# Performance work log

Hardware: AMD Instinct MI355X
Metric: run time of the kernel (lower is better)

The kernel has to match this reference:

```python
import jax, jax.numpy as jnp
import numpy as np

N_ENTRIES = 4_194_304   # total CSR entries (gene observations)
H, W = 256, 256
N_PIXELS = H * W
N_GENES = 30000
FEATURE_DIM = 64


def setup_inputs() -> dict:
    key = jax.random.key(0)
    k1, k2, k3, k4 = jax.random.split(key, 4)
    # gene id per CSR entry
    indices = jax.random.randint(k1, (N_ENTRIES,), 0, N_GENES, dtype=jnp.int64)
    # counts per entry (positive floats)
    cnts = jax.random.uniform(k2, (N_ENTRIES,), dtype=jnp.float32) * 10.0
    # CSR row pointers over pixels: sorted, starting at 0, ending at N_ENTRIES
    indptr = jnp.sort(jax.random.randint(k3, (N_PIXELS + 1,), 0, N_ENTRIES + 1, dtype=jnp.int64))
    indptr = indptr.at[0].set(0).at[-1].set(N_ENTRIES)
    # params: gamma init zeros, tokens variance_scaling(1.0,'fan_in','normal',out_axis=0)
    gamma = jnp.zeros((N_GENES,), jnp.float32)
    tokens = jax.random.normal(k4, (N_GENES, FEATURE_DIM), dtype=jnp.float32) * (1.0 / np.sqrt(FEATURE_DIM))
    return {"indices": indices, "cnts": cnts, "indptr": indptr, "gamma": gamma, "tokens": tokens}


def reference(indices, cnts, indptr, gamma, tokens):
    # SGStem with rescale=True, normalize=False (module defaults)
    n_entries = indices.shape[0]
    n_pixels = indptr.shape[0] - 1  # == H*W
    # mask padding entries beyond indptr[-1]
    valid = jnp.arange(n_entries) < indptr[-1]
    c = jnp.where(valid, cnts, 0.0)
    # rescale counts by per-gene exp(gamma)
    c = c * jnp.exp(gamma[indices])
    # CSR -> segment ids per entry
    rpt = jnp.diff(indptr)
    segms = jnp.repeat(jnp.arange(n_pixels), rpt, total_repeat_length=n_entries)
    # gather token embeddings, scale, scatter-add into pixel bins
    embeddings = tokens[indices] * c[:, None]  # (n_entries, feature_dim)
    embedding_sum = jax.ops.segment_sum(embeddings, segms, num_segments=n_pixels)
    return embedding_sum.reshape(H, W, tokens.shape[-1])
```

## Files before the change

kernel.cpp:

```cpp
#include <hip/hip_runtime.h>
#include <hip/hip_bf16.h>

#define FDIM 64
#define N_PIXELS 65536
#define N_ENTRIES 4194304
#define EPW 512
#define N_WAVES (N_ENTRIES / EPW)
#define PAD 64

typedef unsigned int u32;
typedef u32 u32x4 __attribute__((ext_vector_type(4)));

__device__ __forceinline__ unsigned short f32_to_bf16_rne(float f) {
    unsigned int u = __float_as_uint(f);
    u = (u + 0x7FFFu + ((u >> 16) & 1u)) >> 16;
    return (unsigned short)u;
}

__global__ __launch_bounds__(256) void convert_tokens(
    const float4* __restrict__ tokens4,
    const float* __restrict__ gamma,
    ushort4* __restrict__ tok_bf)
{
    const int i = blockIdx.x * blockDim.x + threadIdx.x;
    const int g = i >> 4;
    const float eg = __expf(gamma[g]);
    const float4 t = tokens4[i];
    ushort4 o;
    o.x = f32_to_bf16_rne(t.x * eg);
    o.y = f32_to_bf16_rne(t.y * eg);
    o.z = f32_to_bf16_rne(t.z * eg);
    o.w = f32_to_bf16_rne(t.w * eg);
    tok_bf[i] = o;
}

__global__ __launch_bounds__(64) void search_starts(
    const int* __restrict__ indptr,
    int* __restrict__ p0arr)
{
    const int w = blockIdx.x * 64 + threadIdx.x;
    const int e0 = w * EPW;
    int lo = 0, hi = N_PIXELS;
    while (lo < hi) {
        const int mid = (lo + hi + 1) >> 1;
        if (indptr[mid] <= e0) lo = mid; else hi = mid - 1;
    }
    p0arr[w] = lo;
}

__global__ __launch_bounds__(64, 4) void sgstem_main(
    const int* __restrict__ indices,
    const float* __restrict__ cnts,
    const int* __restrict__ indptr,
    const char* __restrict__ tokp,
    const int* __restrict__ p0arr,
    float* __restrict__ out)
{
    __shared__ int2 meta[EPW + PAD];

    const int lane = threadIdx.x;
    const int g    = lane >> 3;
    const int fl   = lane & 7;
    const int flb  = fl * 16;

    const int wid = __builtin_amdgcn_readfirstlane(blockIdx.x);
    const int e0 = wid * EPW;
    const int e1 = e0 + EPW;

    #pragma unroll
    for (int c = 0; c < EPW / 64; ++c) {
        const int e = e0 + c * 64 + lane;
        const int   idx = indices[e];
        const float cnt = cnts[e];
        meta[c * 64 + lane] = make_int2(idx * 128, __float_as_int(cnt));
    }
    meta[EPW + lane] = make_int2(0, 0);

    int p = p0arr[wid];

    #define GLOAD(dst, off) \
        asm volatile("global_load_dwordx4 %0, %1, %2" \
                     : "=v"(dst) : "v"(off), "s"(tokp) : "memory")
    #define CONSUME(tk, sc) \
        a0 = fmaf(__uint_as_float(tk.x << 16),         sc, a0); \
        a1 = fmaf(__uint_as_float(tk.x & 0xFFFF0000u), sc, a1); \
        a2 = fmaf(__uint_as_float(tk.y << 16),         sc, a2); \
        a3 = fmaf(__uint_as_float(tk.y & 0xFFFF0000u), sc, a3); \
        a4 = fmaf(__uint_as_float(tk.z << 16),         sc, a4); \
        a5 = fmaf(__uint_as_float(tk.z & 0xFFFF0000u), sc, a5); \
        a6 = fmaf(__uint_as_float(tk.w << 16),         sc, a6); \
        a7 = fmaf(__uint_as_float(tk.w & 0xFFFF0000u), sc, a7)

    while (p < N_PIXELS) {
        const int ps = indptr[p];
        if (ps >= e1) break;
        const int pe = indptr[p + 1];
        const int s = max(ps, e0);
        const int t = min(pe, e1);

        if (t > s) {
            const int r0 = s - e0;
            const int r1 = t - e0;

            float a0 = 0.f, a1 = 0.f, a2 = 0.f, a3 = 0.f;
            float a4 = 0.f, a5 = 0.f, a6 = 0.f, a7 = 0.f;

            int rb = r0;
            for (; rb + 64 <= r1; rb += 64) {
                const int q = rb + g;
                const int2 m0 = meta[q];
                const int2 m1 = meta[q + 8];
                const int2 m2 = meta[q + 16];
                const int2 m3 = meta[q + 24];
                const int2 m4 = meta[q + 32];
                const int2 m5 = meta[q + 40];
                const int2 m6 = meta[q + 48];
                const int2 m7 = meta[q + 56];

                u32x4 t0, t1, t2, t3, t4, t5, t6, t7;
                GLOAD(t0, m0.x + flb); GLOAD(t1, m1.x + flb);
                GLOAD(t2, m2.x + flb); GLOAD(t3, m3.x + flb);
                GLOAD(t4, m4.x + flb); GLOAD(t5, m5.x + flb);
                GLOAD(t6, m6.x + flb); GLOAD(t7, m7.x + flb);

                const float s0 = __int_as_float(m0.y);
                const float s1 = __int_as_float(m1.y);
                const float s2 = __int_as_float(m2.y);
                const float s3 = __int_as_float(m3.y);
                const float s4 = __int_as_float(m4.y);
                const float s5 = __int_as_float(m5.y);
                const float s6 = __int_as_float(m6.y);
                const float s7 = __int_as_float(m7.y);

                asm volatile("s_waitcnt vmcnt(4)" ::: "memory");
                __builtin_amdgcn_sched_barrier(0);
                CONSUME(t0, s0); CONSUME(t1, s1); CONSUME(t2, s2); CONSUME(t3, s3);
                asm volatile("s_waitcnt vmcnt(0)" ::: "memory");
                __builtin_amdgcn_sched_barrier(0);
                CONSUME(t4, s4); CONSUME(t5, s5); CONSUME(t6, s6); CONSUME(t7, s7);
            }

            if (rb < r1) {
                const int q = rb + g;
                const int2 m0 = meta[q];
                const int2 m1 = meta[q + 8];
                const int2 m2 = meta[q + 16];
                const int2 m3 = meta[q + 24];
                const int2 m4 = meta[q + 32];
                const int2 m5 = meta[q + 40];
                const int2 m6 = meta[q + 48];
                const int2 m7 = meta[q + 56];

                const int o0 = ((q      < r1) ? m0.x : 0) + flb;
                const int o1 = ((q +  8 < r1) ? m1.x : 0) + flb;
                const int o2 = ((q + 16 < r1) ? m2.x : 0) + flb;
                const int o3 = ((q + 24 < r1) ? m3.x : 0) + flb;
                const int o4 = ((q + 32 < r1) ? m4.x : 0) + flb;
                const int o5 = ((q + 40 < r1) ? m5.x : 0) + flb;
                const int o6 = ((q + 48 < r1) ? m6.x : 0) + flb;
                const int o7 = ((q + 56 < r1) ? m7.x : 0) + flb;

                u32x4 t0, t1, t2, t3, t4, t5, t6, t7;
                GLOAD(t0, o0); GLOAD(t1, o1); GLOAD(t2, o2); GLOAD(t3, o3);
                GLOAD(t4, o4); GLOAD(t5, o5); GLOAD(t6, o6); GLOAD(t7, o7);

                const float s0 = (q      < r1) ? __int_as_float(m0.y) : 0.f;
                const float s1 = (q +  8 < r1) ? __int_as_float(m1.y) : 0.f;
                const float s2 = (q + 16 < r1) ? __int_as_float(m2.y) : 0.f;
                const float s3 = (q + 24 < r1) ? __int_as_float(m3.y) : 0.f;
                const float s4 = (q + 32 < r1) ? __int_as_float(m4.y) : 0.f;
                const float s5 = (q + 40 < r1) ? __int_as_float(m5.y) : 0.f;
                const float s6 = (q + 48 < r1) ? __int_as_float(m6.y) : 0.f;
                const float s7 = (q + 56 < r1) ? __int_as_float(m7.y) : 0.f;

                asm volatile("s_waitcnt vmcnt(4)" ::: "memory");
                __builtin_amdgcn_sched_barrier(0);
                CONSUME(t0, s0); CONSUME(t1, s1); CONSUME(t2, s2); CONSUME(t3, s3);
                asm volatile("s_waitcnt vmcnt(0)" ::: "memory");
                __builtin_amdgcn_sched_barrier(0);
                CONSUME(t4, s4); CONSUME(t5, s5); CONSUME(t6, s6); CONSUME(t7, s7);
            }

            #pragma unroll
            for (int mask = 8; mask <= 32; mask <<= 1) {
                a0 += __shfl_xor(a0, mask);
                a1 += __shfl_xor(a1, mask);
                a2 += __shfl_xor(a2, mask);
                a3 += __shfl_xor(a3, mask);
                a4 += __shfl_xor(a4, mask);
                a5 += __shfl_xor(a5, mask);
                a6 += __shfl_xor(a6, mask);
                a7 += __shfl_xor(a7, mask);
            }

            if (g == 0) {
                const bool interior = (ps >= e0) && (pe <= e1);
                if (interior) {
                    float4* o4 = (float4*)(out + p * FDIM);
                    o4[fl * 2]     = make_float4(a0, a1, a2, a3);
                    o4[fl * 2 + 1] = make_float4(a4, a5, a6, a7);
                } else {
                    float* o = out + p * FDIM + fl * 8;
                    atomicAdd(o + 0, a0);
                    atomicAdd(o + 1, a1);
                    atomicAdd(o + 2, a2);
                    atomicAdd(o + 3, a3);
                    atomicAdd(o + 4, a4);
                    atomicAdd(o + 5, a5);
                    atomicAdd(o + 6, a6);
                    atomicAdd(o + 7, a7);
                }
            }
        }
        ++p;
    }
    #undef GLOAD
    #undef CONSUME
}

extern "C" void kernel_launch(void* const* d_in, const int* in_sizes, int n_in,
                              void* d_out, int out_size, void* d_ws, size_t ws_size,
                              hipStream_t stream) {
    const int*    indices = (const int*)d_in[0];
    const float*  cnts    = (const float*)d_in[1];
    const int*    indptr  = (const int*)d_in[2];
    const float*  gamma   = (const float*)d_in[3];
    const float4* tokens4 = (const float4*)d_in[4];
    float*        out     = (float*)d_out;

    int*     p0arr  = (int*)d_ws;
    ushort4* tok_bf = (ushort4*)((char*)d_ws + 32768);

    hipMemsetAsync(d_out, 0, (size_t)N_PIXELS * FDIM * sizeof(float), stream);

    convert_tokens<<<1875, 256, 0, stream>>>(tokens4, gamma, tok_bf);
    search_starts<<<N_WAVES / 64, 64, 0, stream>>>(indptr, p0arr);

    sgstem_main<<<N_WAVES, 64, 0, stream>>>(
        indices, cnts, indptr, (const char*)tok_bf, p0arr, out);
}
```

Baseline: 153.1 us.

## Software-pipeline token gathers across chunks and pixels with double-buffered register sets

Restructures the per-wave loop into a flat chunk stream, where each chunk is up to 64 entries of one pixel. Two register sets (A/B) are used so the next chunk's eight gather loads are issued before the current chunk is consumed, including across pixel boundaries. The aim is to hide global-load latency that the old per-pixel loop exposed at each pixel's start. The cost is doubled register use for loaded tokens, which may lower occupancy, plus more complex control flow.

```diff
diff --git a/kernel.cpp b/kernel.cpp
--- a/kernel.cpp
+++ b/kernel.cpp
@@ -70,17 +70,59 @@
     #pragma unroll
     for (int c = 0; c < EPW / 64; ++c) {
         const int e = e0 + c * 64 + lane;
-        const int   idx = indices[e];
-        const float cnt = cnts[e];
-        meta[c * 64 + lane] = make_int2(idx * 128, __float_as_int(cnt));
+        meta[c * 64 + lane] = make_int2(indices[e] * 128, __float_as_int(cnts[e]));
     }
     meta[EPW + lane] = make_int2(0, 0);
 
-    int p = p0arr[wid];
+    int cp = p0arr[wid], cps = 0, cpe = 0, crb = 0, cr1 = 0;
+    {
+        bool found = false;
+        while (cp < N_PIXELS) {
+            const int ps = indptr[cp];
+            if (ps >= e1) break;
+            const int pe = indptr[cp + 1];
+            const int s = max(ps, e0), t = min(pe, e1);
+            if (t > s) { cps = ps; cpe = pe; crb = s - e0; cr1 = t - e0; found = true; break; }
+            ++cp;
+        }
+        if (!found) return;
+    }
+
+    u32x4 tA0, tA1, tA2, tA3, tA4, tA5, tA6, tA7;
+    u32x4 tB0, tB1, tB2, tB3, tB4, tB5, tB6, tB7;
+    float sA0, sA1, sA2, sA3, sA4, sA5, sA6, sA7;
+    float sB0, sB1, sB2, sB3, sB4, sB5, sB6, sB7;
+    float a0 = 0.f, a1 = 0.f, a2 = 0.f, a3 = 0.f;
+    float a4 = 0.f, a5 = 0.f, a6 = 0.f, a7 = 0.f;
 
     #define GLOAD(dst, off) \
         asm volatile("global_load_dwordx4 %0, %1, %2" \
                      : "=v"(dst) : "v"(off), "s"(tokp) : "memory")
+
+    #define ISSUE(SET, RB, R1) do { \
+        const int q_ = (RB) + g; \
+        const int2 m0_ = meta[q_];      const int2 m1_ = meta[q_ + 8]; \
+        const int2 m2_ = meta[q_ + 16]; const int2 m3_ = meta[q_ + 24]; \
+        const int2 m4_ = meta[q_ + 32]; const int2 m5_ = meta[q_ + 40]; \
+        const int2 m6_ = meta[q_ + 48]; const int2 m7_ = meta[q_ + 56]; \
+        GLOAD(t##SET##0, ((q_      < (R1)) ? m0_.x : 0) + flb); \
+        GLOAD(t##SET##1, ((q_ +  8 < (R1)) ? m1_.x : 0) + flb); \
+        GLOAD(t##SET##2, ((q_ + 16 < (R1)) ? m2_.x : 0) + flb); \
+        GLOAD(t##SET##3, ((q_ + 24 < (R1)) ? m3_.x : 0) + flb); \
+        GLOAD(t##SET##4, ((q_ + 32 < (R1)) ? m4_.x : 0) + flb); \
+        GLOAD(t##SET##5, ((q_ + 40 < (R1)) ? m5_.x : 0) + flb); \
+        GLOAD(t##SET##6, ((q_ + 48 < (R1)) ? m6_.x : 0) + flb); \
+        GLOAD(t##SET##7, ((q_ + 56 < (R1)) ? m7_.x : 0) + flb); \
+        s##SET##0 = (q_      < (R1)) ? __int_as_float(m0_.y) : 0.f; \
+        s##SET##1 = (q_ +  8 < (R1)) ? __int_as_float(m1_.y) : 0.f; \
+        s##SET##2 = (q_ + 16 < (R1)) ? __int_as_float(m2_.y) : 0.f; \
+        s##SET##3 = (q_ + 24 < (R1)) ? __int_as_float(m3_.y) : 0.f; \
+        s##SET##4 = (q_ + 32 < (R1)) ? __int_as_float(m4_.y) : 0.f; \
+        s##SET##5 = (q_ + 40 < (R1)) ? __int_as_float(m5_.y) : 0.f; \
+        s##SET##6 = (q_ + 48 < (R1)) ? __int_as_float(m6_.y) : 0.f; \
+        s##SET##7 = (q_ + 56 < (R1)) ? __int_as_float(m7_.y) : 0.f; \
+    } while (0)
+
     #define CONSUME(tk, sc) \
         a0 = fmaf(__uint_as_float(tk.x << 16),         sc, a0); \
         a1 = fmaf(__uint_as_float(tk.x & 0xFFFF0000u), sc, a1); \
@@ -91,131 +133,93 @@
         a6 = fmaf(__uint_as_float(tk.w << 16),         sc, a6); \
         a7 = fmaf(__uint_as_float(tk.w & 0xFFFF0000u), sc, a7)
 
-    while (p < N_PIXELS) {
-        const int ps = indptr[p];
-        if (ps >= e1) break;
-        const int pe = indptr[p + 1];
-        const int s = max(ps, e0);
-        const int t = min(pe, e1);
-
-        if (t > s) {
-            const int r0 = s - e0;
-            const int r1 = t - e0;
-
-            float a0 = 0.f, a1 = 0.f, a2 = 0.f, a3 = 0.f;
-            float a4 = 0.f, a5 = 0.f, a6 = 0.f, a7 = 0.f;
-
-            int rb = r0;
-            for (; rb + 64 <= r1; rb += 64) {
-                const int q = rb + g;
-                const int2 m0 = meta[q];
-                const int2 m1 = meta[q + 8];
-                const int2 m2 = meta[q + 16];
-                const int2 m3 = meta[q + 24];
-                const int2 m4 = meta[q + 32];
-                const int2 m5 = meta[q + 40];
-                const int2 m6 = meta[q + 48];
-                const int2 m7 = meta[q + 56];
-
-                u32x4 t0, t1, t2, t3, t4, t5, t6, t7;
-                GLOAD(t0, m0.x + flb); GLOAD(t1, m1.x + flb);
-                GLOAD(t2, m2.x + flb); GLOAD(t3, m3.x + flb);
-                GLOAD(t4, m4.x + flb); GLOAD(t5, m5.x + flb);
-                GLOAD(t6, m6.x + flb); GLOAD(t7, m7.x + flb);
-
-                const float s0 = __int_as_float(m0.y);
-                const float s1 = __int_as_float(m1.y);
-                const float s2 = __int_as_float(m2.y);
-                const float s3 = __int_as_float(m3.y);
-                const float s4 = __int_as_float(m4.y);
-                const float s5 = __int_as_float(m5.y);
-                const float s6 = __int_as_float(m6.y);
-                const float s7 = __int_as_float(m7.y);
-
-                asm volatile("s_waitcnt vmcnt(4)" ::: "memory");
-                __builtin_amdgcn_sched_barrier(0);
-                CONSUME(t0, s0); CONSUME(t1, s1); CONSUME(t2, s2); CONSUME(t3, s3);
-                asm volatile("s_waitcnt vmcnt(0)" ::: "memory");
-                __builtin_amdgcn_sched_barrier(0);
-                CONSUME(t4, s4); CONSUME(t5, s5); CONSUME(t6, s6); CONSUME(t7, s7);
-            }
-
-            if (rb < r1) {
-                const int q = rb + g;
-                const int2 m0 = meta[q];
-                const int2 m1 = meta[q + 8];
-                const int2 m2 = meta[q + 16];
-                const int2 m3 = meta[q + 24];
-                const int2 m4 = meta[q + 32];
-                const int2 m5 = meta[q + 40];
-                const int2 m6 = meta[q + 48];
-                const int2 m7 = meta[q + 56];
-
-                const int o0 = ((q      < r1) ? m0.x : 0) + flb;
-                const int o1 = ((q +  8 < r1) ? m1.x : 0) + flb;
-                const int o2 = ((q + 16 < r1) ? m2.x : 0) + flb;
-                const int o3 = ((q + 24 < r1) ? m3.x : 0) + flb;
-                const int o4 = ((q + 32 < r1) ? m4.x : 0) + flb;
-                const int o5 = ((q + 40 < r1) ? m5.x : 0) + flb;
-                const int o6 = ((q + 48 < r1) ? m6.x : 0) + flb;
-                const int o7 = ((q + 56 < r1) ? m7.x : 0) + flb;
-
-                u32x4 t0, t1, t2, t3, t4, t5, t6, t7;
-                GLOAD(t0, o0); GLOAD(t1, o1); GLOAD(t2, o2); GLOAD(t3, o3);
-                GLOAD(t4, o4); GLOAD(t5, o5); GLOAD(t6, o6); GLOAD(t7, o7);
-
-                const float s0 = (q      < r1) ? __int_as_float(m0.y) : 0.f;
-                const float s1 = (q +  8 < r1) ? __int_as_float(m1.y) : 0.f;
-                const float s2 = (q + 16 < r1) ? __int_as_float(m2.y) : 0.f;
-                const float s3 = (q + 24 < r1) ? __int_as_float(m3.y) : 0.f;
-                const float s4 = (q + 32 < r1) ? __int_as_float(m4.y) : 0.f;
-                const float s5 = (q + 40 < r1) ? __int_as_float(m5.y) : 0.f;
-                const float s6 = (q + 48 < r1) ? __int_as_float(m6.y) : 0.f;
-                const float s7 = (q + 56 < r1) ? __int_as_float(m7.y) : 0.f;
-
-                asm volatile("s_waitcnt vmcnt(4)" ::: "memory");
-                __builtin_amdgcn_sched_barrier(0);
-                CONSUME(t0, s0); CONSUME(t1, s1); CONSUME(t2, s2); CONSUME(t3, s3);
-                asm volatile("s_waitcnt vmcnt(0)" ::: "memory");
-                __builtin_amdgcn_sched_barrier(0);
-                CONSUME(t4, s4); CONSUME(t5, s5); CONSUME(t6, s6); CONSUME(t7, s7);
-            }
-
-            #pragma unroll
-            for (int mask = 8; mask <= 32; mask <<= 1) {
-                a0 += __shfl_xor(a0, mask);
-                a1 += __shfl_xor(a1, mask);
-                a2 += __shfl_xor(a2, mask);
-                a3 += __shfl_xor(a3, mask);
-                a4 += __shfl_xor(a4, mask);
-                a5 += __shfl_xor(a5, mask);
-                a6 += __shfl_xor(a6, mask);
-                a7 += __shfl_xor(a7, mask);
-            }
-
-            if (g == 0) {
-                const bool interior = (ps >= e0) && (pe <= e1);
-                if (interior) {
-                    float4* o4 = (float4*)(out + p * FDIM);
-                    o4[fl * 2]     = make_float4(a0, a1, a2, a3);
-                    o4[fl * 2 + 1] = make_float4(a4, a5, a6, a7);
-                } else {
-                    float* o = out + p * FDIM + fl * 8;
-                    atomicAdd(o + 0, a0);
-                    atomicAdd(o + 1, a1);
-                    atomicAdd(o + 2, a2);
-                    atomicAdd(o + 3, a3);
-                    atomicAdd(o + 4, a4);
-                    atomicAdd(o + 5, a5);
-                    atomicAdd(o + 6, a6);
-                    atomicAdd(o + 7, a7);
-                }
-            }
+    #define CONSUME_SET(SET) do { \
+        CONSUME(t##SET##0, s##SET##0); CONSUME(t##SET##1, s##SET##1); \
+        CONSUME(t##SET##2, s##SET##2); CONSUME(t##SET##3, s##SET##3); \
+        CONSUME(t##SET##4, s##SET##4); CONSUME(t##SET##5, s##SET##5); \
+        CONSUME(t##SET##6, s##SET##6); CONSUME(t##SET##7, s##SET##7); \
+    } while (0)
+
+    #define ADVANCE(VALID) do { \
+        VALID = false; \
+        if (crb + 64 < cr1) { crb += 64; VALID = true; } \
+        else { \
+            ++cp; \
+            while (cp < N_PIXELS) { \
+                const int ps_ = indptr[cp]; \
+                if (ps_ >= e1) { cp = N_PIXELS; break; } \
+                const int pe_ = indptr[cp + 1]; \
+                const int s_ = max(ps_, e0); \
+                const int t_ = min(pe_, e1); \
+                if (t_ > s_) { cps = ps_; cpe = pe_; crb = s_ - e0; cr1 = t_ - e0; \
+                               VALID = true; break; } \
+                ++cp; \
+            } \
+        } \
+    } while (0)
+
+    #define FLUSH(DP, DPS, DPE) do { \
+        _Pragma("unroll") \
+        for (int mask_ = 8; mask_ <= 32; mask_ <<= 1) { \
+            a0 += __shfl_xor(a0, mask_); a1 += __shfl_xor(a1, mask_); \
+            a2 += __shfl_xor(a2, mask_); a3 += __shfl_xor(a3, mask_); \
+            a4 += __shfl_xor(a4, mask_); a5 += __shfl_xor(a5, mask_); \
+            a6 += __shfl_xor(a6, mask_); a7 += __shfl_xor(a7, mask_); \
+        } \
+        if (g == 0) { \
+            if ((DPS) >= e0 && (DPE) <= e1) { \
+                float4* o4_ = (float4*)(out + (DP) * FDIM); \
+                o4_[fl * 2]     = make_float4(a0, a1, a2, a3); \
+                o4_[fl * 2 + 1] = make_float4(a4, a5, a6, a7); \
+            } else { \
+                float* o_ = out + (DP) * FDIM + fl * 8; \
+                atomicAdd(o_ + 0, a0); atomicAdd(o_ + 1, a1); \
+                atomicAdd(o_ + 2, a2); atomicAdd(o_ + 3, a3); \
+                atomicAdd(o_ + 4, a4); atomicAdd(o_ + 5, a5); \
+                atomicAdd(o_ + 6, a6); atomicAdd(o_ + 7, a7); \
+            } \
+        } \
+        a0 = a1 = a2 = a3 = 0.f; a4 = a5 = a6 = a7 = 0.f; \
+    } while (0)
+
+    int dp = cp, dps = cps, dpe = cpe, drb = crb, dr1 = cr1;
+    ISSUE(A, crb, cr1);
+
+    bool nv;
+    for (;;) {
+        ADVANCE(nv);
+        if (nv) {
+            ISSUE(B, crb, cr1);
+            asm volatile("s_waitcnt vmcnt(8)" ::: "memory");
+        } else {
+            asm volatile("s_waitcnt vmcnt(0)" ::: "memory");
         }
-        ++p;
-    }
+        __builtin_amdgcn_sched_barrier(0);
+        CONSUME_SET(A);
+        if (drb + 64 >= dr1) FLUSH(dp, dps, dpe);
+        if (!nv) break;
+        dp = cp; dps = cps; dpe = cpe; drb = crb; dr1 = cr1;
+
+        ADVANCE(nv);
+        if (nv) {
+            ISSUE(A, crb, cr1);
+            asm volatile("s_waitcnt vmcnt(8)" ::: "memory");
+        } else {
+            asm volatile("s_waitcnt vmcnt(0)" ::: "memory");
+        }
+        __builtin_amdgcn_sched_barrier(0);
+        CONSUME_SET(B);
+        if (drb + 64 >= dr1) FLUSH(dp, dps, dpe);
+        if (!nv) break;
+        dp = cp; dps = cps; dpe = cpe; drb = crb; dr1 = cr1;
+    }
+
     #undef GLOAD
+    #undef ISSUE
     #undef CONSUME
+    #undef CONSUME_SET
+    #undef ADVANCE
+    #undef FLUSH
 }
 
 extern "C" void kernel_launch(void* const* d_in, const int* in_sizes, int n_in,
```

Measured after the change: 150.9 us. No clear change (-1.4%).
